# Optimization experiments

Measured on AMD Instinct MI355X. Metric: run time of the kernel, lower is better.

The kernel has to match this reference:

```python
import jax, jax.numpy as jnp
import numpy as np

N_SETS, N_POINTS, D_FEAT = 8, 4096, 16
K = 16


def setup_inputs() -> dict:
    key = jax.random.key(0)
    x = jax.random.normal(key, (N_SETS, N_POINTS, D_FEAT), dtype=jnp.float32)
    return {"x": x, "k": K}


def reference(x, k):
    """Faithful kNN-graph construction.

    x: (N, M, D) point sets. Returns (src, dst) flattened edge lists with
    per-sample node-ID offsets (node j of set i -> global id i*M + j), plus
    the top-k squared distances (the selection values).
    """
    n_samples, n_points, _ = x.shape
    # pairwise squared distance: ||xi||^2 + ||xj||^2 - 2 xi.xj  -> (N, M, M)
    x2s = jnp.sum(x * x, axis=-1, keepdims=True)
    dist = x2s + jnp.swapaxes(x2s, -1, -2) - 2.0 * jnp.einsum("nmd,npd->nmp", x, x)
    # k smallest distances per row (argtopk descending=False)
    neg_vals, k_indices = jax.lax.top_k(-dist, k)            # (N, M, k)
    topk_dist = -neg_vals
    per_sample_offset = (jnp.arange(n_samples, dtype=jnp.int32) * n_points)[:, None, None]
    dst = k_indices.astype(jnp.int32) + per_sample_offset     # neighbor ids
    src = jnp.broadcast_to(
        jnp.arange(n_points, dtype=jnp.int32)[None, :, None], k_indices.shape
    ) + per_sample_offset                                     # query ids
    return src.reshape(-1), dst.reshape(-1), topk_dist
```

## Files before the change

kernel.cpp:

```cpp
#include <hip/hip_runtime.h>

typedef unsigned long long u64;

#define NSETS 8
#define NPTS  4096
#define DF    16
#define KNN   16
#define QPB   64
#define NCH   8
#define BLK   (QPB * NCH)
#define TILE  512
#define NTILE (NPTS / TILE)
#define SLICE (TILE / NCH)
#define NEDGE (NSETS * NPTS * KNN)

#define RES      8
#define FLUSH_AT 5
#define GRP      4

#define FEAT_B   (TILE * DF * 4)
#define NRM_B    (TILE * 4)
#define RESV_OFF (FEAT_B + NRM_B)
#define SMEM_B   (RESV_OFF + RES * BLK * 8)
#define MPAD     17

__device__ __forceinline__ unsigned flip_f(float d) {
    unsigned b = __float_as_uint(d);
    return (b & 0x80000000u) ? ~b : (b | 0x80000000u);
}
__device__ __forceinline__ float unflip_f(unsigned u) {
    unsigned b = (u & 0x80000000u) ? (u ^ 0x80000000u) : ~u;
    return __uint_as_float(b);
}

#define CEB(i, j) { u64 _a = B[i], _b = B[j]; bool _c = _b < _a; \
                    B[i] = _c ? _b : _a; B[j] = _c ? _a : _b; }
#define CEL(i, j) { u64 _a = Lk[i], _b = Lk[j]; bool _c = _b < _a; \
                    Lk[i] = _c ? _b : _a; Lk[j] = _c ? _a : _b; }

__global__ __launch_bounds__(BLK) void knn_kernel(const float* __restrict__ x,
                                                  float* __restrict__ out) {
    __shared__ float tau_sh[QPB];
    __shared__ __align__(16) char smem[SMEM_B];
    float4* feat4 = (float4*)smem;
    float*  nrm_t = (float*)(smem + FEAT_B);
    u64*    resv  = (u64*)(smem + RESV_OFF);
    float*          lds_d = (float*)smem;
    unsigned short* lds_i = (unsigned short*)(smem + BLK * MPAD * 4);

    const int t    = threadIdx.x;
    const int lane = t & 63;
    const int wv   = t >> 6;
    const int set  = blockIdx.x >> 6;
    const int q0   = (blockIdx.x & 63) * QPB;
    const int q    = q0 + lane;

    const float* xs = x + (size_t)set * NPTS * DF;

    if (t < QPB) tau_sh[t] = 3.0e38f;

    float qn[DF];
    float q2;
    {
        const float4* qp = (const float4*)(xs + (size_t)q * DF);
        float4 a = qp[0], b = qp[1], g = qp[2], d = qp[3];
        float r0 = __fadd_rn(__fmul_rn(a.x, a.x), __fmul_rn(g.x, g.x));
        float r1 = __fadd_rn(__fmul_rn(a.y, a.y), __fmul_rn(g.y, g.y));
        float r2 = __fadd_rn(__fmul_rn(a.z, a.z), __fmul_rn(g.z, g.z));
        float r3 = __fadd_rn(__fmul_rn(a.w, a.w), __fmul_rn(g.w, g.w));
        float r4 = __fadd_rn(__fmul_rn(b.x, b.x), __fmul_rn(d.x, d.x));
        float r5 = __fadd_rn(__fmul_rn(b.y, b.y), __fmul_rn(d.y, d.y));
        float r6 = __fadd_rn(__fmul_rn(b.z, b.z), __fmul_rn(d.z, d.z));
        float r7 = __fadd_rn(__fmul_rn(b.w, b.w), __fmul_rn(d.w, d.w));
        q2 = __fadd_rn(__fadd_rn(__fadd_rn(r0, r1), __fadd_rn(r2, r3)),
                       __fadd_rn(__fadd_rn(r4, r5), __fadd_rn(r6, r7)));
        qn[0]=a.x; qn[1]=a.y; qn[2]=a.z; qn[3]=a.w;
        qn[4]=b.x; qn[5]=b.y; qn[6]=b.z; qn[7]=b.w;
        qn[8]=g.x; qn[9]=g.y; qn[10]=g.z; qn[11]=g.w;
        qn[12]=d.x; qn[13]=d.y; qn[14]=d.z; qn[15]=d.w;
#pragma unroll
        for (int d2 = 0; d2 < DF; ++d2) qn[d2] = -2.0f * qn[d2];
    }

    const u64 SENT = ((u64)flip_f(3.0e38f) << 32) | 0xFFFFFFFFull;
    u64   Lk[KNN];
#pragma unroll
    for (int j = 0; j < KNN; ++j) Lk[j] = SENT;
    float tau_reg = 3.0e38f;
    int   cnt = 0;

    auto flush = [&]() {
        u64 B[RES];
#pragma unroll
        for (int e = 0; e < RES; ++e) {
            u64 v = resv[e * BLK + t];
            B[e] = (e < cnt) ? v : SENT;
        }
        CEB(0,1) CEB(2,3) CEB(4,5) CEB(6,7)
        CEB(0,2) CEB(1,3) CEB(4,6) CEB(5,7)
        CEB(1,2) CEB(5,6)
        CEB(0,4) CEB(1,5) CEB(2,6) CEB(3,7)
        CEB(2,4) CEB(3,5)
        CEB(1,2) CEB(3,4) CEB(5,6)
#pragma unroll
        for (int i = 0; i < RES; ++i) {
            u64 a = Lk[KNN - 1 - i], b = B[i];
            Lk[KNN - 1 - i] = (b < a) ? b : a;
        }
        CEL(0,8)  CEL(1,9)  CEL(2,10) CEL(3,11)
        CEL(4,12) CEL(5,13) CEL(6,14) CEL(7,15)
        CEL(0,4)  CEL(1,5)  CEL(2,6)  CEL(3,7)
        CEL(8,12) CEL(9,13) CEL(10,14) CEL(11,15)
        CEL(0,2)  CEL(1,3)  CEL(4,6)  CEL(5,7)
        CEL(8,10) CEL(9,11) CEL(12,14) CEL(13,15)
        CEL(0,1)  CEL(2,3)  CEL(4,5)  CEL(6,7)
        CEL(8,9)  CEL(10,11) CEL(12,13) CEL(14,15)
        cnt = 0;
        const float kth = unflip_f((unsigned)(Lk[KNN - 1] >> 32));
        tau_reg = kth;
        volatile float* ts = (volatile float*)tau_sh;
        float cur = ts[lane];
        ts[lane] = fminf(cur, kth);
    };

    for (int tile = 0; tile < NTILE; ++tile) {
        __syncthreads();
        {
            const int c = tile * TILE + t;
            const float4* p = (const float4*)(xs + (size_t)c * DF);
            float4 a = p[0], b = p[1], g = p[2], d = p[3];
            float r0 = __fadd_rn(__fmul_rn(a.x, a.x), __fmul_rn(g.x, g.x));
            float r1 = __fadd_rn(__fmul_rn(a.y, a.y), __fmul_rn(g.y, g.y));
            float r2 = __fadd_rn(__fmul_rn(a.z, a.z), __fmul_rn(g.z, g.z));
            float r3 = __fadd_rn(__fmul_rn(a.w, a.w), __fmul_rn(g.w, g.w));
            float r4 = __fadd_rn(__fmul_rn(b.x, b.x), __fmul_rn(d.x, d.x));
            float r5 = __fadd_rn(__fmul_rn(b.y, b.y), __fmul_rn(d.y, d.y));
            float r6 = __fadd_rn(__fmul_rn(b.z, b.z), __fmul_rn(d.z, d.z));
            float r7 = __fadd_rn(__fmul_rn(b.w, b.w), __fmul_rn(d.w, d.w));
            feat4[0 * TILE + t] = a;
            feat4[1 * TILE + t] = b;
            feat4[2 * TILE + t] = g;
            feat4[3 * TILE + t] = d;
            nrm_t[t] = __fadd_rn(
                __fadd_rn(__fadd_rn(r0, r1), __fadd_rn(r2, r3)),
                __fadd_rn(__fadd_rn(r4, r5), __fadd_rn(r6, r7)));
        }
        __syncthreads();

        const int lbase = wv * SLICE;
        const int gbase = tile * TILE + lbase;

        for (int g = 0; g < SLICE; g += GRP) {
            const float tsh = ((volatile float*)tau_sh)[lane];
            const float tau = fminf(tsh, tau_reg);
#pragma unroll
            for (int u = 0; u < GRP; ++u) {
                const int lc = lbase + g + u;
                float4 f0 = feat4[0 * TILE + lc];
                float4 f1 = feat4[1 * TILE + lc];
                float4 f2 = feat4[2 * TILE + lc];
                float4 f3 = feat4[3 * TILE + lc];
                const float nc = nrm_t[lc];
                float dot = 0.f;
                dot = fmaf(qn[0],  f0.x, dot); dot = fmaf(qn[1],  f0.y, dot);
                dot = fmaf(qn[2],  f0.z, dot); dot = fmaf(qn[3],  f0.w, dot);
                dot = fmaf(qn[4],  f1.x, dot); dot = fmaf(qn[5],  f1.y, dot);
                dot = fmaf(qn[6],  f1.z, dot); dot = fmaf(qn[7],  f1.w, dot);
                dot = fmaf(qn[8],  f2.x, dot); dot = fmaf(qn[9],  f2.y, dot);
                dot = fmaf(qn[10], f2.z, dot); dot = fmaf(qn[11], f2.w, dot);
                dot = fmaf(qn[12], f3.x, dot); dot = fmaf(qn[13], f3.y, dot);
                dot = fmaf(qn[14], f3.z, dot); dot = fmaf(qn[15], f3.w, dot);
                const float dist = __fadd_rn(__fadd_rn(q2, nc), dot);
                if (dist <= tau) {
                    resv[cnt * BLK + t] =
                        ((u64)flip_f(dist) << 32) | (unsigned)(gbase + g + u);
                    ++cnt;
                }
            }
            if (__any(cnt >= FLUSH_AT)) flush();
        }
    }
    flush();

    __syncthreads();
#pragma unroll
    for (int j = 0; j < KNN; ++j) {
        lds_d[t * MPAD + j] = unflip_f((unsigned)(Lk[j] >> 32));
        lds_i[t * MPAD + j] = (unsigned short)(Lk[j] & 0xFFFFu);
    }
    __syncthreads();

    if (t < QPB) {
        const int l = t;
        float h[NCH];
        int   hi[NCH];
        int   p[NCH];
#pragma unroll
        for (int w2 = 0; w2 < NCH; ++w2) {
            p[w2]  = 0;
            h[w2]  = lds_d[(w2 * QPB + l) * MPAD];
            hi[w2] = (int)lds_i[(w2 * QPB + l) * MPAD];
        }

        const int    gq = set * NPTS + q0 + l;
        const size_t eb = (size_t)gq * KNN;
        float* osrc = out;
        float* odst = out + (size_t)NEDGE;
        float* odis = out + 2 * (size_t)NEDGE;
        const float srcf = (float)gq;

        for (int e = 0; e < KNN; ++e) {
            float best = h[0];
            int   bi   = hi[0];
            int   bw   = 0;
#pragma unroll
            for (int w2 = 1; w2 < NCH; ++w2) {
                const bool better = (h[w2] < best) ||
                                    (h[w2] == best && hi[w2] < bi);
                if (better) { best = h[w2]; bi = hi[w2]; bw = w2; }
            }

#pragma unroll
            for (int w2 = 0; w2 < NCH; ++w2) {
                if (bw == w2) {
                    ++p[w2];
                    if (p[w2] < KNN) {
                        h[w2]  = lds_d[(w2 * QPB + l) * MPAD + p[w2]];
                        hi[w2] = (int)lds_i[(w2 * QPB + l) * MPAD + p[w2]];
                    } else {
                        h[w2]  = 3.0e38f;
                        hi[w2] = 0x7FFFFFFF;
                    }
                }
            }

            osrc[eb + e] = srcf;
            odst[eb + e] = (float)(set * NPTS + bi);
            odis[eb + e] = best;
        }
    }
}

extern "C" void kernel_launch(void* const* d_in, const int* in_sizes, int n_in,
                              void* d_out, int out_size, void* d_ws, size_t ws_size,
                              hipStream_t stream) {
    (void)in_sizes; (void)n_in; (void)out_size; (void)d_ws; (void)ws_size;
    const float* x = (const float*)d_in[0];
    float* out = (float*)d_out;

    knn_kernel<<<NSETS * (NPTS / QPB), BLK, 0, stream>>>(x, out);
}
```

Baseline: 232.3 us.

## Pair candidates in interleaved LDS layout and use packed FMA for distances

```diff
diff --git a/kernel.cpp b/kernel.cpp
--- a/kernel.cpp
+++ b/kernel.cpp
@@ -1,6 +1,8 @@
 #include <hip/hip_runtime.h>
 
 typedef unsigned long long u64;
+typedef float f2 __attribute__((ext_vector_type(2)));
+typedef float f4 __attribute__((ext_vector_type(4)));
 
 #define NSETS 8
 #define NPTS  4096
@@ -12,11 +14,12 @@
 #define TILE  512
 #define NTILE (NPTS / TILE)
 #define SLICE (TILE / NCH)
+#define PAIRS (SLICE / 2)
 #define NEDGE (NSETS * NPTS * KNN)
 
 #define RES      8
 #define FLUSH_AT 5
-#define GRP      4
+#define GRPP     2
 
 #define FEAT_B   (TILE * DF * 4)
 #define NRM_B    (TILE * 4)
@@ -33,6 +36,16 @@
     return __uint_as_float(b);
 }
 
+__device__ __forceinline__ f2 sp2(float v) { f2 r = {v, v}; return r; }
+
+__device__ __forceinline__ f2 fma2(f2 a, f2 b, f2 c) {
+#if __has_builtin(__builtin_elementwise_fma)
+    return __builtin_elementwise_fma(a, b, c);
+#else
+    f2 r; r.x = fmaf(a.x, b.x, c.x); r.y = fmaf(a.y, b.y, c.y); return r;
+#endif
+}
+
 #define CEB(i, j) { u64 _a = B[i], _b = B[j]; bool _c = _b < _a; \
                     B[i] = _c ? _b : _a; B[j] = _c ? _a : _b; }
 #define CEL(i, j) { u64 _a = Lk[i], _b = Lk[j]; bool _c = _b < _a; \
@@ -42,9 +55,9 @@
                                                   float* __restrict__ out) {
     __shared__ float tau_sh[QPB];
     __shared__ __align__(16) char smem[SMEM_B];
-    float4* feat4 = (float4*)smem;
-    float*  nrm_t = (float*)(smem + FEAT_B);
-    u64*    resv  = (u64*)(smem + RESV_OFF);
+    f4*  pf   = (f4*)smem;
+    f2*  nrm2 = (f2*)(smem + FEAT_B);
+    u64* resv = (u64*)(smem + RESV_OFF);
     float*          lds_d = (float*)smem;
     unsigned short* lds_i = (unsigned short*)(smem + BLK * MPAD * 4);
 
@@ -81,6 +94,7 @@
 #pragma unroll
         for (int d2 = 0; d2 < DF; ++d2) qn[d2] = -2.0f * qn[d2];
     }
+    const f2 q22 = sp2(q2);
 
     const u64 SENT = ((u64)flip_f(3.0e38f) << 32) | 0xFFFFFFFFull;
     u64   Lk[KNN];
@@ -137,44 +151,81 @@
             float r5 = __fadd_rn(__fmul_rn(b.y, b.y), __fmul_rn(d.y, d.y));
             float r6 = __fadd_rn(__fmul_rn(b.z, b.z), __fmul_rn(d.z, d.z));
             float r7 = __fadd_rn(__fmul_rn(b.w, b.w), __fmul_rn(d.w, d.w));
-            feat4[0 * TILE + t] = a;
-            feat4[1 * TILE + t] = b;
-            feat4[2 * TILE + t] = g;
-            feat4[3 * TILE + t] = d;
-            nrm_t[t] = __fadd_rn(
+            const int cp  = t >> 1;
+            const int sub = t & 1;
+            float* w0 = (float*)&pf[0 * 256 + cp];
+            float* w1 = (float*)&pf[1 * 256 + cp];
+            float* w2 = (float*)&pf[2 * 256 + cp];
+            float* w3 = (float*)&pf[3 * 256 + cp];
+            float* w4 = (float*)&pf[4 * 256 + cp];
+            float* w5 = (float*)&pf[5 * 256 + cp];
+            float* w6 = (float*)&pf[6 * 256 + cp];
+            float* w7 = (float*)&pf[7 * 256 + cp];
+            w0[sub] = a.x; w0[sub + 2] = a.y;
+            w1[sub] = a.z; w1[sub + 2] = a.w;
+            w2[sub] = b.x; w2[sub + 2] = b.y;
+            w3[sub] = b.z; w3[sub + 2] = b.w;
+            w4[sub] = g.x; w4[sub + 2] = g.y;
+            w5[sub] = g.z; w5[sub + 2] = g.w;
+            w6[sub] = d.x; w6[sub + 2] = d.y;
+            w7[sub] = d.z; w7[sub + 2] = d.w;
+            ((float*)nrm2)[t] = __fadd_rn(
                 __fadd_rn(__fadd_rn(r0, r1), __fadd_rn(r2, r3)),
                 __fadd_rn(__fadd_rn(r4, r5), __fadd_rn(r6, r7)));
         }
         __syncthreads();
 
-        const int lbase = wv * SLICE;
-        const int gbase = tile * TILE + lbase;
-
-        for (int g = 0; g < SLICE; g += GRP) {
+        const int pbase = wv * PAIRS;
+        const int gbase = tile * TILE;
+
+        for (int g = 0; g < PAIRS; g += GRPP) {
             const float tsh = ((volatile float*)tau_sh)[lane];
             const float tau = fminf(tsh, tau_reg);
 #pragma unroll
-            for (int u = 0; u < GRP; ++u) {
-                const int lc = lbase + g + u;
-                float4 f0 = feat4[0 * TILE + lc];
-                float4 f1 = feat4[1 * TILE + lc];
-                float4 f2 = feat4[2 * TILE + lc];
-                float4 f3 = feat4[3 * TILE + lc];
-                const float nc = nrm_t[lc];
-                float dot = 0.f;
-                dot = fmaf(qn[0],  f0.x, dot); dot = fmaf(qn[1],  f0.y, dot);
-                dot = fmaf(qn[2],  f0.z, dot); dot = fmaf(qn[3],  f0.w, dot);
-                dot = fmaf(qn[4],  f1.x, dot); dot = fmaf(qn[5],  f1.y, dot);
-                dot = fmaf(qn[6],  f1.z, dot); dot = fmaf(qn[7],  f1.w, dot);
-                dot = fmaf(qn[8],  f2.x, dot); dot = fmaf(qn[9],  f2.y, dot);
-                dot = fmaf(qn[10], f2.z, dot); dot = fmaf(qn[11], f2.w, dot);
-                dot = fmaf(qn[12], f3.x, dot); dot = fmaf(qn[13], f3.y, dot);
-                dot = fmaf(qn[14], f3.z, dot); dot = fmaf(qn[15], f3.w, dot);
-                const float dist = __fadd_rn(__fadd_rn(q2, nc), dot);
-                if (dist <= tau) {
-                    resv[cnt * BLK + t] =
-                        ((u64)flip_f(dist) << 32) | (unsigned)(gbase + g + u);
-                    ++cnt;
+            for (int u = 0; u < GRPP; ++u) {
+                const int lp = pbase + g + u;
+                const f4* pp = pf + lp;
+                f4 c0 = pp[0 * 256];
+                f4 c1 = pp[1 * 256];
+                f4 c2 = pp[2 * 256];
+                f4 c3 = pp[3 * 256];
+                f4 c4 = pp[4 * 256];
+                f4 c5 = pp[5 * 256];
+                f4 c6 = pp[6 * 256];
+                f4 c7 = pp[7 * 256];
+                const f2 nn = nrm2[lp];
+                f2 acc = {0.f, 0.f};
+                acc = fma2(sp2(qn[0]),  c0.lo, acc);
+                acc = fma2(sp2(qn[1]),  c0.hi, acc);
+                acc = fma2(sp2(qn[2]),  c1.lo, acc);
+                acc = fma2(sp2(qn[3]),  c1.hi, acc);
+                acc = fma2(sp2(qn[4]),  c2.lo, acc);
+                acc = fma2(sp2(qn[5]),  c2.hi, acc);
+                acc = fma2(sp2(qn[6]),  c3.lo, acc);
+                acc = fma2(sp2(qn[7]),  c3.hi, acc);
+                acc = fma2(sp2(qn[8]),  c4.lo, acc);
+                acc = fma2(sp2(qn[9]),  c4.hi, acc);
+                acc = fma2(sp2(qn[10]), c5.lo, acc);
+                acc = fma2(sp2(qn[11]), c5.hi, acc);
+                acc = fma2(sp2(qn[12]), c6.lo, acc);
+                acc = fma2(sp2(qn[13]), c6.hi, acc);
+                acc = fma2(sp2(qn[14]), c7.lo, acc);
+                acc = fma2(sp2(qn[15]), c7.hi, acc);
+                const f2 d2 = (q22 + nn) + acc;
+                const bool iA = d2.x <= tau;
+                const bool iB = d2.y <= tau;
+                if (__any(iA | iB)) {
+                    const int gA = gbase + (lp << 1);
+                    if (iA) {
+                        resv[cnt * BLK + t] =
+                            ((u64)flip_f(d2.x) << 32) | (unsigned)gA;
+                        ++cnt;
+                    }
+                    if (iB) {
+                        resv[cnt * BLK + t] =
+                            ((u64)flip_f(d2.y) << 32) | (unsigned)(gA + 1);
+                        ++cnt;
+                    }
                 }
             }
             if (__any(cnt >= FLUSH_AT)) flush();
```

Measured after the change: 306.4 us. 1.32x slower.
